# Optimization experiments

Measured on AMD Instinct MI355X. Metric: run time of the kernel, lower is better.

## Reference

```python
import jax, jax.numpy as jnp
import numpy as np

N_NODES = 50000
N_EDGES = 800000
IN_FEATS = 96
HIDDEN = 48


def setup_inputs() -> dict:
    key = jax.random.key(0)
    ks = jax.random.split(key, 16)
    x = jax.random.normal(ks[0], (N_NODES, IN_FEATS), dtype=jnp.float32)
    edge_index = jax.random.randint(ks[1], (2, N_EDGES), 0, N_NODES, dtype=jnp.int32)

    def lin(k, fan_in, fan_out):
        s = 1.0 / np.sqrt(fan_in)
        return jax.random.uniform(k, (fan_in, fan_out), jnp.float32, -s, s)

    return {
        "x": x,
        "edge_index": edge_index,
        # SAGEConv layer 0: in -> hidden
        "w_self0": lin(ks[2], IN_FEATS, HIDDEN),
        "w_neigh0": lin(ks[3], IN_FEATS, HIDDEN),
        "b0": jnp.zeros((HIDDEN,), jnp.float32),
        # SAGEConv layer 1: hidden -> hidden
        "w_self1": lin(ks[4], HIDDEN, HIDDEN),
        "w_neigh1": lin(ks[5], HIDDEN, HIDDEN),
        "b1": jnp.zeros((HIDDEN,), jnp.float32),
        # SAGEConv layer 2: hidden -> hidden
        "w_self2": lin(ks[6], HIDDEN, HIDDEN),
        "w_neigh2": lin(ks[7], HIDDEN, HIDDEN),
        "b2": jnp.zeros((HIDDEN,), jnp.float32),
        # prediction head: hidden -> 1
        "w_pred": lin(ks[8], HIDDEN, 1),
        "b_pred": jnp.zeros((1,), jnp.float32),
    }


def _sage_mean(x, src, dst, deg_inv, w_self, w_neigh, b):
    # mean over in-neighbors: gather src features, segment-sum at dst, / in-degree
    agg = jax.ops.segment_sum(x[src], dst, num_segments=N_NODES) * deg_inv  # [N, F]
    return x @ w_self + agg @ w_neigh + b


def reference(x, edge_index, w_self0, w_neigh0, b0, w_self1, w_neigh1, b1,
              w_self2, w_neigh2, b2, w_pred, b_pred):
    src, dst = edge_index[0], edge_index[1]
    deg = jax.ops.segment_sum(jnp.ones((src.shape[0],), x.dtype), dst,
                              num_segments=N_NODES)
    deg_inv = (1.0 / jnp.maximum(deg, 1.0))[:, None]  # isolated nodes -> 0 agg

    h = jax.nn.relu(_sage_mean(x, src, dst, deg_inv, w_self0, w_neigh0, b0))
    h = jax.nn.relu(_sage_mean(h, src, dst, deg_inv, w_self1, w_neigh1, b1))
    h = jax.nn.relu(_sage_mean(h, src, dst, deg_inv, w_self2, w_neigh2, b2))
    return h @ w_pred + b_pred  # [N, 1]
```

## Files before the change

### kernel.cpp

```cpp
#include <hip/hip_runtime.h>


constexpr int HID = 48;
constexpr int MAXDEG = 64;
constexpr int GNB = 64;

__global__ __launch_bounds__(128) void fill_proj_k(
    const float* __restrict__ X, const float* __restrict__ W,
    float* __restrict__ out_p, int n_nodes,
    const int* __restrict__ src, const int* __restrict__ dst,
    int* __restrict__ cnt, unsigned short* __restrict__ buckets,
    int n_edges, int gemm_blocks) {
    __shared__ float wlds[96 * HID];
    const int t = threadIdx.x;

    if ((int)blockIdx.x >= gemm_blocks) {
        int base = (blockIdx.x - gemm_blocks) * 256 + t;
        int e0 = base, e1 = base + 128;
        if (e0 < n_edges) {
            int d = dst[e0];
            int s = src[e0];
            int pos = atomicAdd(&cnt[d], 1);
            if (pos < MAXDEG) buckets[(size_t)d * MAXDEG + pos] = (unsigned short)s;
        }
        if (e1 < n_edges) {
            int d = dst[e1];
            int s = src[e1];
            int pos = atomicAdd(&cnt[d], 1);
            if (pos < MAXDEG) buckets[(size_t)d * MAXDEG + pos] = (unsigned short)s;
        }
        return;
    }

    for (int i = t; i < 96 * HID; i += 128) wlds[i] = W[i];
    __syncthreads();

    const int q = t & 3;
    const int m = t >> 2;
    const int jb = q * 12;
    const int n0 = blockIdx.x * GNB + 2 * m;
    const int n1 = n0 + 1;
    const bool v0 = n0 < n_nodes, v1 = n1 < n_nodes;
    const int cn0 = v0 ? n0 : 0, cn1 = v1 ? n1 : 0;

    float acc0[12], acc1[12];
#pragma unroll
    for (int j = 0; j < 12; ++j) { acc0[j] = 0.0f; acc1[j] = 0.0f; }

    const float4* xr0 = reinterpret_cast<const float4*>(X + (size_t)cn0 * 96);
    const float4* xr1 = reinterpret_cast<const float4*>(X + (size_t)cn1 * 96);
#pragma unroll 4
    for (int k4 = 0; k4 < 24; ++k4) {
        float4 xa = xr0[k4];
        float4 xb = xr1[k4];
#pragma unroll
        for (int c = 0; c < 4; ++c) {
            float xs0 = (c == 0) ? xa.x : (c == 1) ? xa.y : (c == 2) ? xa.z : xa.w;
            float xs1 = (c == 0) ? xb.x : (c == 1) ? xb.y : (c == 2) ? xb.z : xb.w;
            const float4* wr =
                reinterpret_cast<const float4*>(&wlds[(k4 * 4 + c) * HID + jb]);
#pragma unroll
            for (int j4 = 0; j4 < 3; ++j4) {
                float4 wv = wr[j4];
                acc0[j4 * 4 + 0] = fmaf(xs0, wv.x, acc0[j4 * 4 + 0]);
                acc0[j4 * 4 + 1] = fmaf(xs0, wv.y, acc0[j4 * 4 + 1]);
                acc0[j4 * 4 + 2] = fmaf(xs0, wv.z, acc0[j4 * 4 + 2]);
                acc0[j4 * 4 + 3] = fmaf(xs0, wv.w, acc0[j4 * 4 + 3]);
                acc1[j4 * 4 + 0] = fmaf(xs1, wv.x, acc1[j4 * 4 + 0]);
                acc1[j4 * 4 + 1] = fmaf(xs1, wv.y, acc1[j4 * 4 + 1]);
                acc1[j4 * 4 + 2] = fmaf(xs1, wv.z, acc1[j4 * 4 + 2]);
                acc1[j4 * 4 + 3] = fmaf(xs1, wv.w, acc1[j4 * 4 + 3]);
            }
        }
    }
    float4* o0 = reinterpret_cast<float4*>(out_p + (size_t)n0 * HID + jb);
    float4* o1 = reinterpret_cast<float4*>(out_p + (size_t)n1 * HID + jb);
#pragma unroll
    for (int j4 = 0; j4 < 3; ++j4) {
        if (v0) o0[j4] = make_float4(acc0[j4 * 4 + 0], acc0[j4 * 4 + 1],
                                     acc0[j4 * 4 + 2], acc0[j4 * 4 + 3]);
        if (v1) o1[j4] = make_float4(acc1[j4 * 4 + 0], acc1[j4 * 4 + 1],
                                     acc1[j4 * 4 + 2], acc1[j4 * 4 + 3]);
    }
}

__global__ __launch_bounds__(256) void gather_agg_k(const float* __restrict__ p,
                                                    const int* __restrict__ cnt,
                                                    const unsigned short* __restrict__ buckets,
                                                    float* __restrict__ agg, int n_nodes) {
    int gid = blockIdx.x * 256 + threadIdx.x;
    int n = gid / (HID / 4);
    int j4 = gid % (HID / 4);
    if (n >= n_nodes) return;
    int deg = min(cnt[n], MAXDEG);
    const unsigned short* bkt = buckets + (size_t)n * MAXDEG;
    float4 a0 = make_float4(0.f, 0.f, 0.f, 0.f);
    float4 a1 = make_float4(0.f, 0.f, 0.f, 0.f);
    int e = 0;
    for (; e + 4 <= deg; e += 4) {
        int s0 = bkt[e], s1 = bkt[e + 1], s2 = bkt[e + 2], s3 = bkt[e + 3];
        float4 v0 = reinterpret_cast<const float4*>(p + (size_t)s0 * HID)[j4];
        float4 v1 = reinterpret_cast<const float4*>(p + (size_t)s1 * HID)[j4];
        float4 v2 = reinterpret_cast<const float4*>(p + (size_t)s2 * HID)[j4];
        float4 v3 = reinterpret_cast<const float4*>(p + (size_t)s3 * HID)[j4];
        a0.x += v0.x; a0.y += v0.y; a0.z += v0.z; a0.w += v0.w;
        a1.x += v1.x; a1.y += v1.y; a1.z += v1.z; a1.w += v1.w;
        a0.x += v2.x; a0.y += v2.y; a0.z += v2.z; a0.w += v2.w;
        a1.x += v3.x; a1.y += v3.y; a1.z += v3.z; a1.w += v3.w;
    }
    for (; e < deg; ++e) {
        int s0 = bkt[e];
        float4 v0 = reinterpret_cast<const float4*>(p + (size_t)s0 * HID)[j4];
        a0.x += v0.x; a0.y += v0.y; a0.z += v0.z; a0.w += v0.w;
    }
    float di = 1.0f / fmaxf((float)deg, 1.0f);
    reinterpret_cast<float4*>(agg + (size_t)n * HID)[j4] =
        make_float4((a0.x + a1.x) * di, (a0.y + a1.y) * di,
                    (a0.z + a1.z) * di, (a0.w + a1.w) * di);
}

template <int F_IN, bool FUSE, bool HEAD, bool NEXT>
__global__ __launch_bounds__(128) void sage_gemm_k(
    const float* __restrict__ X, const float* __restrict__ W,
    const float* __restrict__ bias, const float* __restrict__ agg,
    const float* __restrict__ w_next, const float* __restrict__ w_pred,
    const float* __restrict__ b_pred, float* __restrict__ out_h,
    float* __restrict__ out_p, int n_nodes) {
    __shared__ float wlds[F_IN * HID];
    __shared__ float wn_lds[NEXT ? HID * HID : 4];
    __shared__ float h_tile[NEXT ? GNB * (HID + 1) : 4];
    __shared__ float bias_lds[HID];
    __shared__ float wpred_lds[HID];

    int t = threadIdx.x;
    for (int i = t; i < F_IN * HID; i += 128) wlds[i] = W[i];
    if (NEXT)
        for (int i = t; i < HID * HID; i += 128) wn_lds[i] = w_next[i];
    if (FUSE && t < HID) bias_lds[t] = bias[t];
    if (HEAD && t < HID) wpred_lds[t] = w_pred[t];
    __syncthreads();

    const int q = t & 3;
    const int m = t >> 2;
    const int jb = q * 12;
    const int n0 = blockIdx.x * GNB + 2 * m;
    const int n1 = n0 + 1;
    const bool v0 = n0 < n_nodes, v1 = n1 < n_nodes;
    const int cn0 = v0 ? n0 : 0, cn1 = v1 ? n1 : 0;

    float acc0[12], acc1[12];
#pragma unroll
    for (int j = 0; j < 12; ++j) {
        float b = FUSE ? bias_lds[jb + j] : 0.0f;
        acc0[j] = b;
        acc1[j] = b;
    }

    const float4* xr0 = reinterpret_cast<const float4*>(X + (size_t)cn0 * F_IN);
    const float4* xr1 = reinterpret_cast<const float4*>(X + (size_t)cn1 * F_IN);
#pragma unroll 4
    for (int k4 = 0; k4 < F_IN / 4; ++k4) {
        float4 xa = xr0[k4];
        float4 xb = xr1[k4];
#pragma unroll
        for (int c = 0; c < 4; ++c) {
            float xs0 = (c == 0) ? xa.x : (c == 1) ? xa.y : (c == 2) ? xa.z : xa.w;
            float xs1 = (c == 0) ? xb.x : (c == 1) ? xb.y : (c == 2) ? xb.z : xb.w;
            const float4* wr =
                reinterpret_cast<const float4*>(&wlds[(k4 * 4 + c) * HID + jb]);
#pragma unroll
            for (int j4 = 0; j4 < 3; ++j4) {
                float4 wv = wr[j4];
                acc0[j4 * 4 + 0] = fmaf(xs0, wv.x, acc0[j4 * 4 + 0]);
                acc0[j4 * 4 + 1] = fmaf(xs0, wv.y, acc0[j4 * 4 + 1]);
                acc0[j4 * 4 + 2] = fmaf(xs0, wv.z, acc0[j4 * 4 + 2]);
                acc0[j4 * 4 + 3] = fmaf(xs0, wv.w, acc0[j4 * 4 + 3]);
                acc1[j4 * 4 + 0] = fmaf(xs1, wv.x, acc1[j4 * 4 + 0]);
                acc1[j4 * 4 + 1] = fmaf(xs1, wv.y, acc1[j4 * 4 + 1]);
                acc1[j4 * 4 + 2] = fmaf(xs1, wv.z, acc1[j4 * 4 + 2]);
                acc1[j4 * 4 + 3] = fmaf(xs1, wv.w, acc1[j4 * 4 + 3]);
            }
        }
    }

    if (FUSE) {
        const float4* a0 = reinterpret_cast<const float4*>(agg + (size_t)cn0 * HID + jb);
        const float4* a1 = reinterpret_cast<const float4*>(agg + (size_t)cn1 * HID + jb);
#pragma unroll
        for (int j4 = 0; j4 < 3; ++j4) {
            float4 av0 = a0[j4];
            float4 av1 = a1[j4];
            acc0[j4 * 4 + 0] += av0.x; acc0[j4 * 4 + 1] += av0.y;
            acc0[j4 * 4 + 2] += av0.z; acc0[j4 * 4 + 3] += av0.w;
            acc1[j4 * 4 + 0] += av1.x; acc1[j4 * 4 + 1] += av1.y;
            acc1[j4 * 4 + 2] += av1.z; acc1[j4 * 4 + 3] += av1.w;
        }
#pragma unroll
        for (int j = 0; j < 12; ++j) {
            acc0[j] = fmaxf(acc0[j], 0.0f);
            acc1[j] = fmaxf(acc1[j], 0.0f);
        }
    }

    if (HEAD) {
        float s0 = 0.0f, s1 = 0.0f;
#pragma unroll
        for (int j = 0; j < 12; ++j) {
            float wp = wpred_lds[jb + j];
            s0 = fmaf(acc0[j], wp, s0);
            s1 = fmaf(acc1[j], wp, s1);
        }
        s0 += __shfl_xor(s0, 1); s0 += __shfl_xor(s0, 2);
        s1 += __shfl_xor(s1, 1); s1 += __shfl_xor(s1, 2);
        if (q == 0) {
            float bp = b_pred[0];
            if (v0) out_h[n0] = s0 + bp;
            if (v1) out_h[n1] = s1 + bp;
        }
        return;
    }

    {
        float4* o0 = reinterpret_cast<float4*>(out_h + (size_t)n0 * HID + jb);
        float4* o1 = reinterpret_cast<float4*>(out_h + (size_t)n1 * HID + jb);
#pragma unroll
        for (int j4 = 0; j4 < 3; ++j4) {
            if (v0) o0[j4] = make_float4(acc0[j4 * 4 + 0], acc0[j4 * 4 + 1],
                                         acc0[j4 * 4 + 2], acc0[j4 * 4 + 3]);
            if (v1) o1[j4] = make_float4(acc1[j4 * 4 + 0], acc1[j4 * 4 + 1],
                                         acc1[j4 * 4 + 2], acc1[j4 * 4 + 3]);
        }
    }

    if (NEXT) {
        const int ln0 = 2 * m, ln1 = 2 * m + 1;
#pragma unroll
        for (int j = 0; j < 12; ++j) {
            h_tile[ln0 * (HID + 1) + jb + j] = acc0[j];
            h_tile[ln1 * (HID + 1) + jb + j] = acc1[j];
        }
        __syncthreads();
        float acc2_0[12], acc2_1[12];
#pragma unroll
        for (int j = 0; j < 12; ++j) { acc2_0[j] = 0.0f; acc2_1[j] = 0.0f; }
#pragma unroll 4
        for (int k = 0; k < HID; ++k) {
            float hs0 = h_tile[ln0 * (HID + 1) + k];
            float hs1 = h_tile[ln1 * (HID + 1) + k];
            const float4* wr = reinterpret_cast<const float4*>(&wn_lds[k * HID + jb]);
#pragma unroll
            for (int j4 = 0; j4 < 3; ++j4) {
                float4 wv = wr[j4];
                acc2_0[j4 * 4 + 0] = fmaf(hs0, wv.x, acc2_0[j4 * 4 + 0]);
                acc2_0[j4 * 4 + 1] = fmaf(hs0, wv.y, acc2_0[j4 * 4 + 1]);
                acc2_0[j4 * 4 + 2] = fmaf(hs0, wv.z, acc2_0[j4 * 4 + 2]);
                acc2_0[j4 * 4 + 3] = fmaf(hs0, wv.w, acc2_0[j4 * 4 + 3]);
                acc2_1[j4 * 4 + 0] = fmaf(hs1, wv.x, acc2_1[j4 * 4 + 0]);
                acc2_1[j4 * 4 + 1] = fmaf(hs1, wv.y, acc2_1[j4 * 4 + 1]);
                acc2_1[j4 * 4 + 2] = fmaf(hs1, wv.z, acc2_1[j4 * 4 + 2]);
                acc2_1[j4 * 4 + 3] = fmaf(hs1, wv.w, acc2_1[j4 * 4 + 3]);
            }
        }
        float4* p0 = reinterpret_cast<float4*>(out_p + (size_t)n0 * HID + jb);
        float4* p1 = reinterpret_cast<float4*>(out_p + (size_t)n1 * HID + jb);
#pragma unroll
        for (int j4 = 0; j4 < 3; ++j4) {
            if (v0) p0[j4] = make_float4(acc2_0[j4 * 4 + 0], acc2_0[j4 * 4 + 1],
                                         acc2_0[j4 * 4 + 2], acc2_0[j4 * 4 + 3]);
            if (v1) p1[j4] = make_float4(acc2_1[j4 * 4 + 0], acc2_1[j4 * 4 + 1],
                                         acc2_1[j4 * 4 + 2], acc2_1[j4 * 4 + 3]);
        }
    }
}

extern "C" void kernel_launch(void* const* d_in, const int* in_sizes, int n_in,
                              void* d_out, int out_size, void* d_ws, size_t ws_size,
                              hipStream_t stream) {
    const float* x        = (const float*)d_in[0];
    const int*   ei       = (const int*)d_in[1];
    const float* w_self0  = (const float*)d_in[2];
    const float* w_neigh0 = (const float*)d_in[3];
    const float* b0       = (const float*)d_in[4];
    const float* w_self1  = (const float*)d_in[5];
    const float* w_neigh1 = (const float*)d_in[6];
    const float* b1       = (const float*)d_in[7];
    const float* w_self2  = (const float*)d_in[8];
    const float* w_neigh2 = (const float*)d_in[9];
    const float* b2       = (const float*)d_in[10];
    const float* w_pred   = (const float*)d_in[11];
    const float* b_pred   = (const float*)d_in[12];

    const int n_nodes = in_sizes[0] / 96;
    const int n_edges = in_sizes[1] / 2;
    const int* src = ei;
    const int* dst = ei + n_edges;

    char* wsb = (char*)d_ws;
    int* cnt                  = (int*)wsb;         wsb += (size_t)n_nodes * 4;
    unsigned short* buckets   = (unsigned short*)wsb; wsb += (size_t)n_nodes * MAXDEG * 2;
    float* p      = (float*)wsb;                   wsb += (size_t)n_nodes * HID * 4;
    float* agg    = (float*)wsb;                   wsb += (size_t)n_nodes * HID * 4;
    float* h      = (float*)wsb;                   wsb += (size_t)n_nodes * HID * 4;
    float* out    = (float*)d_out;

    const int gnb = (n_nodes + GNB - 1) / GNB;
    const int fb = (n_edges + 255) / 256;
    const int ab = (n_nodes * (HID / 4) + 255) / 256;

    hipMemsetAsync(cnt, 0, (size_t)n_nodes * 4, stream);
    fill_proj_k<<<gnb + fb, 128, 0, stream>>>(x, w_neigh0, p, n_nodes,
                                              src, dst, cnt, buckets, n_edges, gnb);

    gather_agg_k<<<ab, 256, 0, stream>>>(p, cnt, buckets, agg, n_nodes);
    sage_gemm_k<96, true, false, true><<<gnb, 128, 0, stream>>>(
        x, w_self0, b0, agg, w_neigh1, nullptr, nullptr, h, p, n_nodes);

    gather_agg_k<<<ab, 256, 0, stream>>>(p, cnt, buckets, agg, n_nodes);
    sage_gemm_k<48, true, false, true><<<gnb, 128, 0, stream>>>(
        h, w_self1, b1, agg, w_neigh2, nullptr, nullptr, h, p, n_nodes);

    gather_agg_k<<<ab, 256, 0, stream>>>(p, cnt, buckets, agg, n_nodes);
    sage_gemm_k<48, true, true, false><<<gnb, 128, 0, stream>>>(
        h, w_self2, b2, agg, nullptr, w_pred, b_pred, out, nullptr, n_nodes);
}
```

Baseline: 255.4 us.

## Fuse neighbor gather into layer kernel and precompute self-projection with bias

The separate gather/aggregate kernel and its agg buffer are removed. The first kernel now computes both the neighbor projection and the self projection plus bias from x, and each later layer kernel gathers neighbor projections, applies mean, adds the self term and ReLU, then computes the next layer's two projections. This cuts the launch count from seven to four and removes the agg write/read round trip. In exchange each thread now gathers 12 contiguous floats per neighbor rather than 4, giving fewer threads in flight for latency hiding during the gather. The extra s buffers add another 48-float store and load per node per layer.

```diff
diff --git a/kernel.cpp b/kernel.cpp
--- a/kernel.cpp
+++ b/kernel.cpp
@@ -6,12 +6,15 @@
 constexpr int GNB = 64;
 
 __global__ __launch_bounds__(128) void fill_proj_k(
-    const float* __restrict__ X, const float* __restrict__ W,
-    float* __restrict__ out_p, int n_nodes,
+    const float* __restrict__ X, const float* __restrict__ Wn,
+    const float* __restrict__ Ws, const float* __restrict__ bias,
+    float* __restrict__ p_out, float* __restrict__ s_out, int n_nodes,
     const int* __restrict__ src, const int* __restrict__ dst,
     int* __restrict__ cnt, unsigned short* __restrict__ buckets,
     int n_edges, int gemm_blocks) {
-    __shared__ float wlds[96 * HID];
+    __shared__ float wn_lds[96 * HID];
+    __shared__ float ws_lds[96 * HID];
+    __shared__ float bias_lds[HID];
     const int t = threadIdx.x;
 
     if ((int)blockIdx.x >= gemm_blocks) {
@@ -32,7 +35,11 @@
         return;
     }
 
-    for (int i = t; i < 96 * HID; i += 128) wlds[i] = W[i];
+    for (int i = t; i < 96 * HID; i += 128) {
+        wn_lds[i] = Wn[i];
+        ws_lds[i] = Ws[i];
+    }
+    if (t < HID) bias_lds[t] = bias[t];
     __syncthreads();
 
     const int q = t & 3;
@@ -43,9 +50,13 @@
     const bool v0 = n0 < n_nodes, v1 = n1 < n_nodes;
     const int cn0 = v0 ? n0 : 0, cn1 = v1 ? n1 : 0;
 
-    float acc0[12], acc1[12];
-#pragma unroll
-    for (int j = 0; j < 12; ++j) { acc0[j] = 0.0f; acc1[j] = 0.0f; }
+    float pa[12], pb[12], sa[12], sb[12];
+#pragma unroll
+    for (int j = 0; j < 12; ++j) {
+        pa[j] = 0.0f; pb[j] = 0.0f;
+        float b = bias_lds[jb + j];
+        sa[j] = b; sb[j] = b;
+    }
 
     const float4* xr0 = reinterpret_cast<const float4*>(X + (size_t)cn0 * 96);
     const float4* xr1 = reinterpret_cast<const float4*>(X + (size_t)cn1 * 96);
@@ -55,89 +66,107 @@
         float4 xb = xr1[k4];
 #pragma unroll
         for (int c = 0; c < 4; ++c) {
-            float xs0 = (c == 0) ? xa.x : (c == 1) ? xa.y : (c == 2) ? xa.z : xa.w;
-            float xs1 = (c == 0) ? xb.x : (c == 1) ? xb.y : (c == 2) ? xb.z : xb.w;
-            const float4* wr =
-                reinterpret_cast<const float4*>(&wlds[(k4 * 4 + c) * HID + jb]);
+            float x0 = (c == 0) ? xa.x : (c == 1) ? xa.y : (c == 2) ? xa.z : xa.w;
+            float x1 = (c == 0) ? xb.x : (c == 1) ? xb.y : (c == 2) ? xb.z : xb.w;
+            const float4* wnr =
+                reinterpret_cast<const float4*>(&wn_lds[(k4 * 4 + c) * HID + jb]);
+            const float4* wsr =
+                reinterpret_cast<const float4*>(&ws_lds[(k4 * 4 + c) * HID + jb]);
 #pragma unroll
             for (int j4 = 0; j4 < 3; ++j4) {
-                float4 wv = wr[j4];
-                acc0[j4 * 4 + 0] = fmaf(xs0, wv.x, acc0[j4 * 4 + 0]);
-                acc0[j4 * 4 + 1] = fmaf(xs0, wv.y, acc0[j4 * 4 + 1]);
-                acc0[j4 * 4 + 2] = fmaf(xs0, wv.z, acc0[j4 * 4 + 2]);
-                acc0[j4 * 4 + 3] = fmaf(xs0, wv.w, acc0[j4 * 4 + 3]);
-                acc1[j4 * 4 + 0] = fmaf(xs1, wv.x, acc1[j4 * 4 + 0]);
-                acc1[j4 * 4 + 1] = fmaf(xs1, wv.y, acc1[j4 * 4 + 1]);
-                acc1[j4 * 4 + 2] = fmaf(xs1, wv.z, acc1[j4 * 4 + 2]);
-                acc1[j4 * 4 + 3] = fmaf(xs1, wv.w, acc1[j4 * 4 + 3]);
+                float4 wv = wnr[j4];
+                pa[j4 * 4 + 0] = fmaf(x0, wv.x, pa[j4 * 4 + 0]);
+                pa[j4 * 4 + 1] = fmaf(x0, wv.y, pa[j4 * 4 + 1]);
+                pa[j4 * 4 + 2] = fmaf(x0, wv.z, pa[j4 * 4 + 2]);
+                pa[j4 * 4 + 3] = fmaf(x0, wv.w, pa[j4 * 4 + 3]);
+                pb[j4 * 4 + 0] = fmaf(x1, wv.x, pb[j4 * 4 + 0]);
+                pb[j4 * 4 + 1] = fmaf(x1, wv.y, pb[j4 * 4 + 1]);
+                pb[j4 * 4 + 2] = fmaf(x1, wv.z, pb[j4 * 4 + 2]);
+                pb[j4 * 4 + 3] = fmaf(x1, wv.w, pb[j4 * 4 + 3]);
+                float4 uv = wsr[j4];
+                sa[j4 * 4 + 0] = fmaf(x0, uv.x, sa[j4 * 4 + 0]);
+                sa[j4 * 4 + 1] = fmaf(x0, uv.y, sa[j4 * 4 + 1]);
+                sa[j4 * 4 + 2] = fmaf(x0, uv.z, sa[j4 * 4 + 2]);
+                sa[j4 * 4 + 3] = fmaf(x0, uv.w, sa[j4 * 4 + 3]);
+                sb[j4 * 4 + 0] = fmaf(x1, uv.x, sb[j4 * 4 + 0]);
+                sb[j4 * 4 + 1] = fmaf(x1, uv.y, sb[j4 * 4 + 1]);
+                sb[j4 * 4 + 2] = fmaf(x1, uv.z, sb[j4 * 4 + 2]);
+                sb[j4 * 4 + 3] = fmaf(x1, uv.w, sb[j4 * 4 + 3]);
             }
         }
     }
-    float4* o0 = reinterpret_cast<float4*>(out_p + (size_t)n0 * HID + jb);
-    float4* o1 = reinterpret_cast<float4*>(out_p + (size_t)n1 * HID + jb);
+    float4* po0 = reinterpret_cast<float4*>(p_out + (size_t)n0 * HID + jb);
+    float4* po1 = reinterpret_cast<float4*>(p_out + (size_t)n1 * HID + jb);
+    float4* so0 = reinterpret_cast<float4*>(s_out + (size_t)n0 * HID + jb);
+    float4* so1 = reinterpret_cast<float4*>(s_out + (size_t)n1 * HID + jb);
 #pragma unroll
     for (int j4 = 0; j4 < 3; ++j4) {
-        if (v0) o0[j4] = make_float4(acc0[j4 * 4 + 0], acc0[j4 * 4 + 1],
-                                     acc0[j4 * 4 + 2], acc0[j4 * 4 + 3]);
-        if (v1) o1[j4] = make_float4(acc1[j4 * 4 + 0], acc1[j4 * 4 + 1],
-                                     acc1[j4 * 4 + 2], acc1[j4 * 4 + 3]);
+        if (v0) {
+            po0[j4] = make_float4(pa[j4 * 4 + 0], pa[j4 * 4 + 1], pa[j4 * 4 + 2], pa[j4 * 4 + 3]);
+            so0[j4] = make_float4(sa[j4 * 4 + 0], sa[j4 * 4 + 1], sa[j4 * 4 + 2], sa[j4 * 4 + 3]);
+        }
+        if (v1) {
+            po1[j4] = make_float4(pb[j4 * 4 + 0], pb[j4 * 4 + 1], pb[j4 * 4 + 2], pb[j4 * 4 + 3]);
+            so1[j4] = make_float4(sb[j4 * 4 + 0], sb[j4 * 4 + 1], sb[j4 * 4 + 2], sb[j4 * 4 + 3]);
+        }
     }
 }
 
-__global__ __launch_bounds__(256) void gather_agg_k(const float* __restrict__ p,
-                                                    const int* __restrict__ cnt,
-                                                    const unsigned short* __restrict__ buckets,
-                                                    float* __restrict__ agg, int n_nodes) {
-    int gid = blockIdx.x * 256 + threadIdx.x;
-    int n = gid / (HID / 4);
-    int j4 = gid % (HID / 4);
-    if (n >= n_nodes) return;
-    int deg = min(cnt[n], MAXDEG);
-    const unsigned short* bkt = buckets + (size_t)n * MAXDEG;
-    float4 a0 = make_float4(0.f, 0.f, 0.f, 0.f);
-    float4 a1 = make_float4(0.f, 0.f, 0.f, 0.f);
+__device__ __forceinline__ void gather12(const float* __restrict__ p_in,
+                                         const unsigned short* __restrict__ bkt,
+                                         int deg, int jb, float4 (&g)[3]) {
+    float4 ga0 = make_float4(0.f, 0.f, 0.f, 0.f), ga1 = ga0, ga2 = ga0;
+    float4 gb0 = ga0, gb1 = ga0, gb2 = ga0;
     int e = 0;
-    for (; e + 4 <= deg; e += 4) {
-        int s0 = bkt[e], s1 = bkt[e + 1], s2 = bkt[e + 2], s3 = bkt[e + 3];
-        float4 v0 = reinterpret_cast<const float4*>(p + (size_t)s0 * HID)[j4];
-        float4 v1 = reinterpret_cast<const float4*>(p + (size_t)s1 * HID)[j4];
-        float4 v2 = reinterpret_cast<const float4*>(p + (size_t)s2 * HID)[j4];
-        float4 v3 = reinterpret_cast<const float4*>(p + (size_t)s3 * HID)[j4];
-        a0.x += v0.x; a0.y += v0.y; a0.z += v0.z; a0.w += v0.w;
-        a1.x += v1.x; a1.y += v1.y; a1.z += v1.z; a1.w += v1.w;
-        a0.x += v2.x; a0.y += v2.y; a0.z += v2.z; a0.w += v2.w;
-        a1.x += v3.x; a1.y += v3.y; a1.z += v3.z; a1.w += v3.w;
-    }
-    for (; e < deg; ++e) {
-        int s0 = bkt[e];
-        float4 v0 = reinterpret_cast<const float4*>(p + (size_t)s0 * HID)[j4];
-        a0.x += v0.x; a0.y += v0.y; a0.z += v0.z; a0.w += v0.w;
-    }
-    float di = 1.0f / fmaxf((float)deg, 1.0f);
-    reinterpret_cast<float4*>(agg + (size_t)n * HID)[j4] =
-        make_float4((a0.x + a1.x) * di, (a0.y + a1.y) * di,
-                    (a0.z + a1.z) * di, (a0.w + a1.w) * di);
+    for (; e + 2 <= deg; e += 2) {
+        int s0 = bkt[e], s1 = bkt[e + 1];
+        const float4* r0 = reinterpret_cast<const float4*>(p_in + (size_t)s0 * HID + jb);
+        const float4* r1 = reinterpret_cast<const float4*>(p_in + (size_t)s1 * HID + jb);
+        float4 a0 = r0[0], a1 = r0[1], a2 = r0[2];
+        float4 b0 = r1[0], b1 = r1[1], b2 = r1[2];
+        ga0.x += a0.x; ga0.y += a0.y; ga0.z += a0.z; ga0.w += a0.w;
+        ga1.x += a1.x; ga1.y += a1.y; ga1.z += a1.z; ga1.w += a1.w;
+        ga2.x += a2.x; ga2.y += a2.y; ga2.z += a2.z; ga2.w += a2.w;
+        gb0.x += b0.x; gb0.y += b0.y; gb0.z += b0.z; gb0.w += b0.w;
+        gb1.x += b1.x; gb1.y += b1.y; gb1.z += b1.z; gb1.w += b1.w;
+        gb2.x += b2.x; gb2.y += b2.y; gb2.z += b2.z; gb2.w += b2.w;
+    }
+    if (e < deg) {
+        const float4* r0 = reinterpret_cast<const float4*>(p_in + (size_t)bkt[e] * HID + jb);
+        float4 a0 = r0[0], a1 = r0[1], a2 = r0[2];
+        ga0.x += a0.x; ga0.y += a0.y; ga0.z += a0.z; ga0.w += a0.w;
+        ga1.x += a1.x; ga1.y += a1.y; ga1.z += a1.z; ga1.w += a1.w;
+        ga2.x += a2.x; ga2.y += a2.y; ga2.z += a2.z; ga2.w += a2.w;
+    }
+    g[0] = make_float4(ga0.x + gb0.x, ga0.y + gb0.y, ga0.z + gb0.z, ga0.w + gb0.w);
+    g[1] = make_float4(ga1.x + gb1.x, ga1.y + gb1.y, ga1.z + gb1.z, ga1.w + gb1.w);
+    g[2] = make_float4(ga2.x + gb2.x, ga2.y + gb2.y, ga2.z + gb2.z, ga2.w + gb2.w);
 }
 
-template <int F_IN, bool FUSE, bool HEAD, bool NEXT>
-__global__ __launch_bounds__(128) void sage_gemm_k(
-    const float* __restrict__ X, const float* __restrict__ W,
-    const float* __restrict__ bias, const float* __restrict__ agg,
-    const float* __restrict__ w_next, const float* __restrict__ w_pred,
-    const float* __restrict__ b_pred, float* __restrict__ out_h,
-    float* __restrict__ out_p, int n_nodes) {
-    __shared__ float wlds[F_IN * HID];
-    __shared__ float wn_lds[NEXT ? HID * HID : 4];
-    __shared__ float h_tile[NEXT ? GNB * (HID + 1) : 4];
-    __shared__ float bias_lds[HID];
+template <bool LAST>
+__global__ __launch_bounds__(128) void fused_layer_k(
+    const float* __restrict__ p_in, const float* __restrict__ s_in,
+    const int* __restrict__ cnt, const unsigned short* __restrict__ buckets,
+    const float* __restrict__ wn_next, const float* __restrict__ ws_next,
+    const float* __restrict__ b_next, const float* __restrict__ w_pred,
+    const float* __restrict__ b_pred, float* __restrict__ p_out,
+    float* __restrict__ s_out, float* __restrict__ out, int n_nodes) {
+    __shared__ float wn_lds[LAST ? 4 : HID * HID];
+    __shared__ float ws_lds[LAST ? 4 : HID * HID];
+    __shared__ float bn_lds[HID];
+    __shared__ float h_tile[LAST ? 4 : GNB * (HID + 1)];
     __shared__ float wpred_lds[HID];
 
-    int t = threadIdx.x;
-    for (int i = t; i < F_IN * HID; i += 128) wlds[i] = W[i];
-    if (NEXT)
-        for (int i = t; i < HID * HID; i += 128) wn_lds[i] = w_next[i];
-    if (FUSE && t < HID) bias_lds[t] = bias[t];
-    if (HEAD && t < HID) wpred_lds[t] = w_pred[t];
+    const int t = threadIdx.x;
+    if (!LAST) {
+        for (int i = t; i < HID * HID; i += 128) {
+            wn_lds[i] = wn_next[i];
+            ws_lds[i] = ws_next[i];
+        }
+        if (t < HID) bn_lds[t] = b_next[t];
+    } else {
+        if (t < HID) wpred_lds[t] = w_pred[t];
+    }
     __syncthreads();
 
     const int q = t & 3;
@@ -148,127 +177,106 @@
     const bool v0 = n0 < n_nodes, v1 = n1 < n_nodes;
     const int cn0 = v0 ? n0 : 0, cn1 = v1 ? n1 : 0;
 
-    float acc0[12], acc1[12];
-#pragma unroll
-    for (int j = 0; j < 12; ++j) {
-        float b = FUSE ? bias_lds[jb + j] : 0.0f;
-        acc0[j] = b;
-        acc1[j] = b;
-    }
-
-    const float4* xr0 = reinterpret_cast<const float4*>(X + (size_t)cn0 * F_IN);
-    const float4* xr1 = reinterpret_cast<const float4*>(X + (size_t)cn1 * F_IN);
-#pragma unroll 4
-    for (int k4 = 0; k4 < F_IN / 4; ++k4) {
-        float4 xa = xr0[k4];
-        float4 xb = xr1[k4];
-#pragma unroll
-        for (int c = 0; c < 4; ++c) {
-            float xs0 = (c == 0) ? xa.x : (c == 1) ? xa.y : (c == 2) ? xa.z : xa.w;
-            float xs1 = (c == 0) ? xb.x : (c == 1) ? xb.y : (c == 2) ? xb.z : xb.w;
-            const float4* wr =
-                reinterpret_cast<const float4*>(&wlds[(k4 * 4 + c) * HID + jb]);
-#pragma unroll
-            for (int j4 = 0; j4 < 3; ++j4) {
-                float4 wv = wr[j4];
-                acc0[j4 * 4 + 0] = fmaf(xs0, wv.x, acc0[j4 * 4 + 0]);
-                acc0[j4 * 4 + 1] = fmaf(xs0, wv.y, acc0[j4 * 4 + 1]);
-                acc0[j4 * 4 + 2] = fmaf(xs0, wv.z, acc0[j4 * 4 + 2]);
-                acc0[j4 * 4 + 3] = fmaf(xs0, wv.w, acc0[j4 * 4 + 3]);
-                acc1[j4 * 4 + 0] = fmaf(xs1, wv.x, acc1[j4 * 4 + 0]);
-                acc1[j4 * 4 + 1] = fmaf(xs1, wv.y, acc1[j4 * 4 + 1]);
-                acc1[j4 * 4 + 2] = fmaf(xs1, wv.z, acc1[j4 * 4 + 2]);
-                acc1[j4 * 4 + 3] = fmaf(xs1, wv.w, acc1[j4 * 4 + 3]);
-            }
-        }
-    }
-
-    if (FUSE) {
-        const float4* a0 = reinterpret_cast<const float4*>(agg + (size_t)cn0 * HID + jb);
-        const float4* a1 = reinterpret_cast<const float4*>(agg + (size_t)cn1 * HID + jb);
-#pragma unroll
-        for (int j4 = 0; j4 < 3; ++j4) {
-            float4 av0 = a0[j4];
-            float4 av1 = a1[j4];
-            acc0[j4 * 4 + 0] += av0.x; acc0[j4 * 4 + 1] += av0.y;
-            acc0[j4 * 4 + 2] += av0.z; acc0[j4 * 4 + 3] += av0.w;
-            acc1[j4 * 4 + 0] += av1.x; acc1[j4 * 4 + 1] += av1.y;
-            acc1[j4 * 4 + 2] += av1.z; acc1[j4 * 4 + 3] += av1.w;
-        }
-#pragma unroll
-        for (int j = 0; j < 12; ++j) {
-            acc0[j] = fmaxf(acc0[j], 0.0f);
-            acc1[j] = fmaxf(acc1[j], 0.0f);
-        }
-    }
-
-    if (HEAD) {
+    const int d0 = min(cnt[cn0], MAXDEG);
+    const int d1 = min(cnt[cn1], MAXDEG);
+    const float di0 = 1.0f / fmaxf((float)d0, 1.0f);
+    const float di1 = 1.0f / fmaxf((float)d1, 1.0f);
+
+    float4 g0[3], g1[3];
+    gather12(p_in, buckets + (size_t)cn0 * MAXDEG, d0, jb, g0);
+    gather12(p_in, buckets + (size_t)cn1 * MAXDEG, d1, jb, g1);
+
+    const float4* sr0 = reinterpret_cast<const float4*>(s_in + (size_t)cn0 * HID + jb);
+    const float4* sr1 = reinterpret_cast<const float4*>(s_in + (size_t)cn1 * HID + jb);
+    float h0v[12], h1v[12];
+#pragma unroll
+    for (int j4 = 0; j4 < 3; ++j4) {
+        float4 sv0 = sr0[j4];
+        float4 sv1 = sr1[j4];
+        h0v[j4 * 4 + 0] = fmaxf(fmaf(di0, g0[j4].x, sv0.x), 0.0f);
+        h0v[j4 * 4 + 1] = fmaxf(fmaf(di0, g0[j4].y, sv0.y), 0.0f);
+        h0v[j4 * 4 + 2] = fmaxf(fmaf(di0, g0[j4].z, sv0.z), 0.0f);
+        h0v[j4 * 4 + 3] = fmaxf(fmaf(di0, g0[j4].w, sv0.w), 0.0f);
+        h1v[j4 * 4 + 0] = fmaxf(fmaf(di1, g1[j4].x, sv1.x), 0.0f);
+        h1v[j4 * 4 + 1] = fmaxf(fmaf(di1, g1[j4].y, sv1.y), 0.0f);
+        h1v[j4 * 4 + 2] = fmaxf(fmaf(di1, g1[j4].z, sv1.z), 0.0f);
+        h1v[j4 * 4 + 3] = fmaxf(fmaf(di1, g1[j4].w, sv1.w), 0.0f);
+    }
+
+    if (LAST) {
         float s0 = 0.0f, s1 = 0.0f;
 #pragma unroll
         for (int j = 0; j < 12; ++j) {
             float wp = wpred_lds[jb + j];
-            s0 = fmaf(acc0[j], wp, s0);
-            s1 = fmaf(acc1[j], wp, s1);
+            s0 = fmaf(h0v[j], wp, s0);
+            s1 = fmaf(h1v[j], wp, s1);
         }
         s0 += __shfl_xor(s0, 1); s0 += __shfl_xor(s0, 2);
         s1 += __shfl_xor(s1, 1); s1 += __shfl_xor(s1, 2);
         if (q == 0) {
             float bp = b_pred[0];
-            if (v0) out_h[n0] = s0 + bp;
-            if (v1) out_h[n1] = s1 + bp;
+            if (v0) out[n0] = s0 + bp;
+            if (v1) out[n1] = s1 + bp;
         }
         return;
     }
 
-    {
-        float4* o0 = reinterpret_cast<float4*>(out_h + (size_t)n0 * HID + jb);
-        float4* o1 = reinterpret_cast<float4*>(out_h + (size_t)n1 * HID + jb);
+    const int ln0 = 2 * m, ln1 = 2 * m + 1;
+#pragma unroll
+    for (int j = 0; j < 12; ++j) {
+        h_tile[ln0 * (HID + 1) + jb + j] = h0v[j];
+        h_tile[ln1 * (HID + 1) + jb + j] = h1v[j];
+    }
+    __syncthreads();
+
+    float pa[12], pb[12], sa[12], sb[12];
+#pragma unroll
+    for (int j = 0; j < 12; ++j) {
+        pa[j] = 0.0f; pb[j] = 0.0f;
+        float b = bn_lds[jb + j];
+        sa[j] = b; sb[j] = b;
+    }
+#pragma unroll 4
+    for (int k = 0; k < HID; ++k) {
+        float ha = h_tile[ln0 * (HID + 1) + k];
+        float hb = h_tile[ln1 * (HID + 1) + k];
+        const float4* wnr = reinterpret_cast<const float4*>(&wn_lds[k * HID + jb]);
+        const float4* wsr = reinterpret_cast<const float4*>(&ws_lds[k * HID + jb]);
 #pragma unroll
         for (int j4 = 0; j4 < 3; ++j4) {
-            if (v0) o0[j4] = make_float4(acc0[j4 * 4 + 0], acc0[j4 * 4 + 1],
-                                         acc0[j4 * 4 + 2], acc0[j4 * 4 + 3]);
-            if (v1) o1[j4] = make_float4(acc1[j4 * 4 + 0], acc1[j4 * 4 + 1],
-                                         acc1[j4 * 4 + 2], acc1[j4 * 4 + 3]);
-        }
-    }
-
-    if (NEXT) {
-        const int ln0 = 2 * m, ln1 = 2 * m + 1;
-#pragma unroll
-        for (int j = 0; j < 12; ++j) {
-            h_tile[ln0 * (HID + 1) + jb + j] = acc0[j];
-            h_tile[ln1 * (HID + 1) + jb + j] = acc1[j];
-        }
-        __syncthreads();
-        float acc2_0[12], acc2_1[12];
-#pragma unroll
-        for (int j = 0; j < 12; ++j) { acc2_0[j] = 0.0f; acc2_1[j] = 0.0f; }
-#pragma unroll 4
-        for (int k = 0; k < HID; ++k) {
-            float hs0 = h_tile[ln0 * (HID + 1) + k];
-            float hs1 = h_tile[ln1 * (HID + 1) + k];
-            const float4* wr = reinterpret_cast<const float4*>(&wn_lds[k * HID + jb]);
-#pragma unroll
-            for (int j4 = 0; j4 < 3; ++j4) {
-                float4 wv = wr[j4];
-                acc2_0[j4 * 4 + 0] = fmaf(hs0, wv.x, acc2_0[j4 * 4 + 0]);
-                acc2_0[j4 * 4 + 1] = fmaf(hs0, wv.y, acc2_0[j4 * 4 + 1]);
-                acc2_0[j4 * 4 + 2] = fmaf(hs0, wv.z, acc2_0[j4 * 4 + 2]);
-                acc2_0[j4 * 4 + 3] = fmaf(hs0, wv.w, acc2_0[j4 * 4 + 3]);
-                acc2_1[j4 * 4 + 0] = fmaf(hs1, wv.x, acc2_1[j4 * 4 + 0]);
-                acc2_1[j4 * 4 + 1] = fmaf(hs1, wv.y, acc2_1[j4 * 4 + 1]);
-                acc2_1[j4 * 4 + 2] = fmaf(hs1, wv.z, acc2_1[j4 * 4 + 2]);
-                acc2_1[j4 * 4 + 3] = fmaf(hs1, wv.w, acc2_1[j4 * 4 + 3]);
-            }
-        }
-        float4* p0 = reinterpret_cast<float4*>(out_p + (size_t)n0 * HID + jb);
-        float4* p1 = reinterpret_cast<float4*>(out_p + (size_t)n1 * HID + jb);
-#pragma unroll
-        for (int j4 = 0; j4 < 3; ++j4) {
-            if (v0) p0[j4] = make_float4(acc2_0[j4 * 4 + 0], acc2_0[j4 * 4 + 1],
-                                         acc2_0[j4 * 4 + 2], acc2_0[j4 * 4 + 3]);
-            if (v1) p1[j4] = make_float4(acc2_1[j4 * 4 + 0], acc2_1[j4 * 4 + 1],
-                                         acc2_1[j4 * 4 + 2], acc2_1[j4 * 4 + 3]);
+            float4 wv = wnr[j4];
+            pa[j4 * 4 + 0] = fmaf(ha, wv.x, pa[j4 * 4 + 0]);
+            pa[j4 * 4 + 1] = fmaf(ha, wv.y, pa[j4 * 4 + 1]);
+            pa[j4 * 4 + 2] = fmaf(ha, wv.z, pa[j4 * 4 + 2]);
+            pa[j4 * 4 + 3] = fmaf(ha, wv.w, pa[j4 * 4 + 3]);
+            pb[j4 * 4 + 0] = fmaf(hb, wv.x, pb[j4 * 4 + 0]);
+            pb[j4 * 4 + 1] = fmaf(hb, wv.y, pb[j4 * 4 + 1]);
+            pb[j4 * 4 + 2] = fmaf(hb, wv.z, pb[j4 * 4 + 2]);
+            pb[j4 * 4 + 3] = fmaf(hb, wv.w, pb[j4 * 4 + 3]);
+            float4 uv = wsr[j4];
+            sa[j4 * 4 + 0] = fmaf(ha, uv.x, sa[j4 * 4 + 0]);
+            sa[j4 * 4 + 1] = fmaf(ha, uv.y, sa[j4 * 4 + 1]);
+            sa[j4 * 4 + 2] = fmaf(ha, uv.z, sa[j4 * 4 + 2]);
+            sa[j4 * 4 + 3] = fmaf(ha, uv.w, sa[j4 * 4 + 3]);
+            sb[j4 * 4 + 0] = fmaf(hb, uv.x, sb[j4 * 4 + 0]);
+            sb[j4 * 4 + 1] = fmaf(hb, uv.y, sb[j4 * 4 + 1]);
+            sb[j4 * 4 + 2] = fmaf(hb, uv.z, sb[j4 * 4 + 2]);
+            sb[j4 * 4 + 3] = fmaf(hb, uv.w, sb[j4 * 4 + 3]);
+        }
+    }
+    float4* po0 = reinterpret_cast<float4*>(p_out + (size_t)n0 * HID + jb);
+    float4* po1 = reinterpret_cast<float4*>(p_out + (size_t)n1 * HID + jb);
+    float4* so0 = reinterpret_cast<float4*>(s_out + (size_t)n0 * HID + jb);
+    float4* so1 = reinterpret_cast<float4*>(s_out + (size_t)n1 * HID + jb);
+#pragma unroll
+    for (int j4 = 0; j4 < 3; ++j4) {
+        if (v0) {
+            po0[j4] = make_float4(pa[j4 * 4 + 0], pa[j4 * 4 + 1], pa[j4 * 4 + 2], pa[j4 * 4 + 3]);
+            so0[j4] = make_float4(sa[j4 * 4 + 0], sa[j4 * 4 + 1], sa[j4 * 4 + 2], sa[j4 * 4 + 3]);
+        }
+        if (v1) {
+            po1[j4] = make_float4(pb[j4 * 4 + 0], pb[j4 * 4 + 1], pb[j4 * 4 + 2], pb[j4 * 4 + 3]);
+            so1[j4] = make_float4(sb[j4 * 4 + 0], sb[j4 * 4 + 1], sb[j4 * 4 + 2], sb[j4 * 4 + 3]);
         }
     }
 }
@@ -296,30 +304,32 @@
     const int* dst = ei + n_edges;
 
     char* wsb = (char*)d_ws;
-    int* cnt                  = (int*)wsb;         wsb += (size_t)n_nodes * 4;
-    unsigned short* buckets   = (unsigned short*)wsb; wsb += (size_t)n_nodes * MAXDEG * 2;
-    float* p      = (float*)wsb;                   wsb += (size_t)n_nodes * HID * 4;
-    float* agg    = (float*)wsb;                   wsb += (size_t)n_nodes * HID * 4;
-    float* h      = (float*)wsb;                   wsb += (size_t)n_nodes * HID * 4;
-    float* out    = (float*)d_out;
+    int* cnt                = (int*)wsb;              wsb += (size_t)n_nodes * 4;
+    unsigned short* buckets = (unsigned short*)wsb;   wsb += (size_t)n_nodes * MAXDEG * 2;
+    float* pA = (float*)wsb;                          wsb += (size_t)n_nodes * HID * 4;
+    float* sA = (float*)wsb;                          wsb += (size_t)n_nodes * HID * 4;
+    float* pB = (float*)wsb;                          wsb += (size_t)n_nodes * HID * 4;
+    float* sB = (float*)wsb;                          wsb += (size_t)n_nodes * HID * 4;
+    float* out = (float*)d_out;
 
     const int gnb = (n_nodes + GNB - 1) / GNB;
     const int fb = (n_edges + 255) / 256;
-    const int ab = (n_nodes * (HID / 4) + 255) / 256;
 
     hipMemsetAsync(cnt, 0, (size_t)n_nodes * 4, stream);
-    fill_proj_k<<<gnb + fb, 128, 0, stream>>>(x, w_neigh0, p, n_nodes,
-                                              src, dst, cnt, buckets, n_edges, gnb);
-
-    gather_agg_k<<<ab, 256, 0, stream>>>(p, cnt, buckets, agg, n_nodes);
-    sage_gemm_k<96, true, false, true><<<gnb, 128, 0, stream>>>(
-        x, w_self0, b0, agg, w_neigh1, nullptr, nullptr, h, p, n_nodes);
-
-    gather_agg_k<<<ab, 256, 0, stream>>>(p, cnt, buckets, agg, n_nodes);
-    sage_gemm_k<48, true, false, true><<<gnb, 128, 0, stream>>>(
-        h, w_self1, b1, agg, w_neigh2, nullptr, nullptr, h, p, n_nodes);
-
-    gather_agg_k<<<ab, 256, 0, stream>>>(p, cnt, buckets, agg, n_nodes);
-    sage_gemm_k<48, true, true, false><<<gnb, 128, 0, stream>>>(
-        h, w_self2, b2, agg, nullptr, w_pred, b_pred, out, nullptr, n_nodes);
+
+    fill_proj_k<<<gnb + fb, 128, 0, stream>>>(x, w_neigh0, w_self0, b0, pA, sA,
+                                              n_nodes, src, dst, cnt, buckets,
+                                              n_edges, gnb);
+    fused_layer_k<false><<<gnb, 128, 0, stream>>>(pA, sA, cnt, buckets,
+                                                  w_neigh1, w_self1, b1,
+                                                  nullptr, nullptr, pB, sB,
+                                                  nullptr, n_nodes);
+    fused_layer_k<false><<<gnb, 128, 0, stream>>>(pB, sB, cnt, buckets,
+                                                  w_neigh2, w_self2, b2,
+                                                  nullptr, nullptr, pA, sA,
+                                                  nullptr, n_nodes);
+    fused_layer_k<true><<<gnb, 128, 0, stream>>>(pA, sA, cnt, buckets,
+                                                 nullptr, nullptr, nullptr,
+                                                 w_pred, b_pred, nullptr,
+                                                 nullptr, out, n_nodes);
 }
```

New measurement: 244.4 us. 1.05x faster.
